# Kernel tuning notes

Measured on AMD Instinct MI355X. Metric: run time of the kernel, lower is better.

## Reference

```python
import jax, jax.numpy as jnp
import numpy as np

H = W = 256          # full-res feature map (2h x 2w)
WIN = 16             # window size
STRIDE = 2           # shifted-window stride
HEADS = 8
DIM_HEAD = 64
INNER = HEADS * DIM_HEAD
DIM = 128
KEEP = 50            # min(int(0.7*(256//16)**2), 50)
IOU_THR = 0.2


def _make_windows():
    xs = np.arange(0, W - WIN + 1, STRIDE)
    ys = np.arange(0, H - WIN + 1, STRIDE)
    gx, gy = np.meshgrid(xs, ys)
    return np.stack([gx.ravel(), gy.ravel(), gx.ravel() + WIN - 1, gy.ravel() + WIN - 1], axis=1)

_WIN_NP = _make_windows()          # [M,4] = (x1,y1,x2,y2), M = 121*121 = 14641
BOXES = jnp.asarray(_WIN_NP, dtype=jnp.float32)
SXY = jnp.asarray(_WIN_NP[:, :2], dtype=jnp.int32)   # integer (sx, sy) origins

# torchvision roi_align (spatial_scale=1, sampling_ratio->ceil(15/16)=1, aligned=False):
_off = (np.arange(WIN) + 0.5) * (WIN - 1.0) / WIN
LO = jnp.asarray(np.floor(_off).astype(np.int32))      # low integer index, in [0,14]
FR = jnp.asarray((_off - np.floor(_off)).astype(np.float32))


def _nms_keep(scores):
    """Greedy NMS over the fixed window grid; returns top-KEEP kept indices."""
    x1, y1, x2, y2 = BOXES[:, 0], BOXES[:, 1], BOXES[:, 2], BOXES[:, 3]
    area = (x2 - x1) * (y2 - y1)

    def body(k, carry):
        live, keep = carry
        idx = jnp.argmax(jnp.where(live, scores, -jnp.inf))
        bb = BOXES[idx]
        iw = jnp.clip(jnp.minimum(x2, bb[2]) - jnp.maximum(x1, bb[0]), 0.0)
        ih = jnp.clip(jnp.minimum(y2, bb[3]) - jnp.maximum(y1, bb[1]), 0.0)
        inter = iw * ih
        iou = inter / (area + area[idx] - inter)
        live = live & (iou <= IOU_THR)
        return live, keep.at[k].set(idx.astype(jnp.int32))

    _, keep = jax.lax.fori_loop(
        0, KEEP, body,
        (jnp.ones(BOXES.shape[0], bool), jnp.zeros(KEEP, jnp.int32)))
    return keep


def _forward(x, prob, fix_w, w_qkv, w_out, b_out):
    b = prob.shape[0]
    d = x.shape[-1]
    # entropy map at half res
    entropy = -jnp.sum(prob * jnp.log2(prob + 1e-10), axis=1)          # [b,128,128]
    # FixCNN: 8x8 ones-init conv, VALID -> [b,1,121,121]; normalized window score
    score = jax.lax.conv_general_dilated(
        entropy[:, None], fix_w, (1, 1), 'VALID',
        dimension_numbers=('NCHW', 'OIHW', 'NCHW'))
    score = score.reshape(b, -1) / float((WIN // 2) * (WIN // 2))      # [b,14641]

    keep = jax.lax.stop_gradient(jax.vmap(_nms_keep)(score))           # [b,KEEP]
    sx = SXY[keep][..., 0]                                             # [b,KEEP]
    sy = SXY[keep][..., 1]

    x2d = x.reshape(b, H, W, d)   # token n = h*W + w (channels-last layout)
    ar = jnp.arange(WIN)

    def gather_one(xi, syi, sxi):  # xi [H,W,d]
        R = syi[:, None, None] + ar[None, :, None]
        C = sxi[:, None, None] + ar[None, None, :]
        return xi[R, C]

    crops = jax.vmap(gather_one)(x2d, sy, sx)                          # [b,K,16,16,d]

    # roi_align bilinear sampling with fixed fractional grid
    c00 = crops[:, :, LO[:, None], LO[None, :]]
    c01 = crops[:, :, LO[:, None], LO[None, :] + 1]
    c10 = crops[:, :, LO[:, None] + 1, LO[None, :]]
    c11 = crops[:, :, LO[:, None] + 1, LO[None, :] + 1]
    fy = FR[:, None, None]
    fx = FR[None, :, None]
    win = ((1 - fy) * (1 - fx) * c00 + (1 - fy) * fx * c01
           + fy * (1 - fx) * c10 + fy * fx * c11)                      # [b,K,16,16,d]

    toks = win.reshape(b * KEEP, WIN * WIN, d)                         # [m,256,d]
    qkv = toks @ w_qkv.T                                               # [m,256,3*INNER]
    q, k_, v = jnp.split(qkv, 3, axis=-1)

    def to_heads(t):
        return t.reshape(t.shape[0], t.shape[1], HEADS, DIM_HEAD).transpose(0, 2, 1, 3)

    q, k_, v = to_heads(q), to_heads(k_), to_heads(v)
    attn = jax.nn.softmax(jnp.einsum('mhnd,mhkd->mhnk', q, k_) * (DIM_HEAD ** -0.5), axis=-1)
    out = jnp.einsum('mhnk,mhkd->mhnd', attn, v)
    out = out.transpose(0, 2, 1, 3).reshape(b * KEEP, WIN * WIN, INNER)
    out = out @ w_out.T + b_out                                        # [m,256,d]

    # overlap scatter-add + count normalization
    out2d = out.reshape(b, KEEP, WIN, WIN, d)
    bidx = jnp.arange(b)[:, None, None, None]
    Y = sy[:, :, None, None] + ar[None, None, :, None]
    X = sx[:, :, None, None] + ar[None, None, None, :]
    acc = jnp.zeros((b, H, W, d), x.dtype).at[bidx, Y, X].add(out2d)
    cnt = jnp.zeros((b, H, W), x.dtype).at[bidx, Y, X].add(1.0)
    outx = (acc / (cnt[..., None] + 1e-10)).reshape(b, H * W, d)
    return x + outx


def setup_inputs() -> dict:
    key = jax.random.key(0)
    ks = jax.random.split(key, 4)
    b = 4
    x = jax.random.normal(ks[0], (b, H * W, DIM), dtype=jnp.float32)
    prob = jax.random.uniform(ks[1], (b, 2, H // 2, W // 2), dtype=jnp.float32)
    fix_w = jnp.ones((1, 1, WIN // 2, WIN // 2), dtype=jnp.float32)
    w_qkv = jax.random.normal(ks[2], (3 * INNER, DIM), dtype=jnp.float32) * 0.02
    w_out = jax.random.normal(ks[3], (DIM, INNER), dtype=jnp.float32) * 0.02
    b_out = jnp.zeros((DIM,), dtype=jnp.float32)
    return {"x": x, "prob": prob, "fix_w": fix_w, "w_qkv": w_qkv, "w_out": w_out, "b_out": b_out}


def reference(x, prob, fix_w, w_qkv, w_out, b_out):
    return _forward(x, prob, fix_w, w_qkv, w_out, b_out)
```

## Files before the change

kernel.cpp:

```cpp
#include <hip/hip_runtime.h>
#include <math.h>

#define NB 4
#define NWIN 121
#define NBOX (NWIN*NWIN)
#define NKEEP 50
#define HWD 256
#define DIM 128
#define HEADS 8
#define NTOK 256
#define NWTOT (NB*NKEEP)
#define SCPAD 15616

#define OFF_ENT   0
#define OFF_SCORE 65536
#define OFF_KEEP  128128
#define OFF_WQKV  128256
#define OFF_WOUT  226560
#define OFF_TOKBF 259328
#define OFF_PO    3536128
#define WS_FLOATS 6812928

#define KPAD 76
#define VPAD 268
#define KP3 68
#define VP3 132

typedef __attribute__((ext_vector_type(8))) short short8;
typedef __attribute__((ext_vector_type(4))) short short4v;
typedef __attribute__((ext_vector_type(4))) float f32x4;

static __device__ __forceinline__ unsigned short f2bf(float f) {
  union { float f; unsigned u; } v; v.f = f;
  unsigned r = (v.u + 0x7fffu + ((v.u >> 16) & 1u)) >> 16;
  return (unsigned short)r;
}
static __device__ __forceinline__ short4v pk4(f32x4 a) {
  short4v r;
  r[0] = (short)f2bf(a[0]); r[1] = (short)f2bf(a[1]);
  r[2] = (short)f2bf(a[2]); r[3] = (short)f2bf(a[3]);
  return r;
}
static __device__ __forceinline__ short8 ld8_lds(const unsigned short* p) {
  short4v a = *(const short4v*)p;
  short4v b = *(const short4v*)(p + 4);
  short8 r;
  r[0]=a[0]; r[1]=a[1]; r[2]=a[2]; r[3]=a[3];
  r[4]=b[0]; r[5]=b[1]; r[6]=b[2]; r[7]=b[3];
  return r;
}
static __device__ __forceinline__ short8 ld8_g(const unsigned short* p) {
  return *(const short8*)p;
}

template<int CTRL>
static __device__ __forceinline__ float dppmax(float v) {
  union { float f; int i; } a, r; a.f = v;
  r.i = __builtin_amdgcn_update_dpp(a.i, a.i, CTRL, 0xf, 0xf, false);
  return fmaxf(v, r.f);
}
static __device__ __forceinline__ float wavemax(float v) {
  v = dppmax<0x111>(v); v = dppmax<0x112>(v);
  v = dppmax<0x114>(v); v = dppmax<0x118>(v);
  v = dppmax<0x142>(v); v = dppmax<0x143>(v);
  union { float f; int i; } gi, gm; gi.f = v;
  gm.i = __builtin_amdgcn_readlane(gi.i, 63);
  return gm.f;
}

__global__ void k_entropy(const float* __restrict__ prob, float* __restrict__ ent) {
  int idx = blockIdx.x * 256 + threadIdx.x;
  int b = idx >> 14, p = idx & 16383;
  float p0 = prob[(size_t)(b * 2) * 16384 + p];
  float p1 = prob[(size_t)(b * 2 + 1) * 16384 + p];
  ent[idx] = -(p0 * log2f(p0 + 1e-10f) + p1 * log2f(p1 + 1e-10f));
}

__global__ void k_score(const float* __restrict__ ent, const float* __restrict__ fw,
                        float* __restrict__ scp) {
  int gid = blockIdx.x * 256 + threadIdx.x;
  if (gid >= NB * SCPAD) return;
  int b = gid / SCPAD, idx = gid % SCPAD;
  int r = idx >> 7, c = idx & 127;
  float s = -INFINITY;
  if (r < NWIN && c < NWIN) {
    const float* e = ent + b * 16384 + r * 128 + c;
    float a = 0.f;
#pragma unroll
    for (int rr = 0; rr < 8; ++rr)
#pragma unroll
      for (int cc = 0; cc < 8; ++cc)
        a += e[rr * 128 + cc] * fw[rr * 8 + cc];
    s = a * (1.0f / 64.0f);
  }
  scp[b * SCPAD + (r << 7) + (c ^ ((r & 7) << 2))] = s;
}

__global__ void k_nms(const float* __restrict__ scp, int* __restrict__ keep) {
  __shared__ float sc[SCPAD];
  int b = blockIdx.x, l = threadIdx.x;
  const float* src = scp + b * SCPAD;
  for (int cb = 0; cb < 64; cb += 8) {
    f32x4 t[8];
#pragma unroll
    for (int i = 0; i < 8; ++i) {
      int idx = (cb + i) * 256 + l * 4;
      if (idx < SCPAD) t[i] = *(const f32x4*)&src[idx];
    }
#pragma unroll
    for (int i = 0; i < 8; ++i) {
      int idx = (cb + i) * 256 + l * 4;
      if (idx < SCPAD) *(f32x4*)&sc[idx] = t[i];
    }
  }
  float M0 = -INFINITY, M1 = -INFINITY; int C0 = 0, C1 = 0;
#pragma unroll
  for (int slot = 0; slot < 2; ++slot) {
    int r = l + slot * 64;
    if (slot == 1 && r >= NWIN) break;
    int r7 = (r & 7) << 2, rbase = r << 7;
    float bv0=-INFINITY,bv1=-INFINITY,bv2=-INFINITY,bv3=-INFINITY;
    int bc0=0,bc1=0,bc2=0,bc3=0;
    for (int lb = 0; lb < 32; ++lb) {
      f32x4 v = *(const f32x4*)&sc[rbase + ((lb << 2) ^ r7)];
      int c0 = lb << 2;
      if (v[0] > bv0) { bv0 = v[0]; bc0 = c0; }
      if (v[1] > bv1) { bv1 = v[1]; bc1 = c0 + 1; }
      if (v[2] > bv2) { bv2 = v[2]; bc2 = c0 + 2; }
      if (v[3] > bv3) { bv3 = v[3]; bc3 = c0 + 3; }
    }
    float bv = bv0; int bc = bc0;
    if (bv1 > bv || (bv1 == bv && bc1 < bc)) { bv = bv1; bc = bc1; }
    if (bv2 > bv || (bv2 == bv && bc2 < bc)) { bv = bv2; bc = bc2; }
    if (bv3 > bv || (bv3 == bv && bc3 < bc)) { bv = bv3; bc = bc3; }
    if (slot == 0) { M0 = bv; C0 = bc; } else { M1 = bv; C1 = bc; }
  }
  for (int k = 0; k < NKEEP; ++k) {
    float gmax = wavemax(fmaxf(M0, M1));
    unsigned long long b0 = __ballot(M0 == gmax);
    unsigned long long b1 = __ballot(M1 == gmax);
    int R;
    if (b0) R = __ffsll((unsigned long long)b0) - 1;
    else    R = 64 + __ffsll((unsigned long long)b1) - 1;
    int Cc = (R < 64) ? __builtin_amdgcn_readlane(C0, R)
                      : __builtin_amdgcn_readlane(C1, R - 64);
    if (l == 0) {
      keep[(b * NKEEP + k) * 2 + 0] = 2 * R;
      keep[(b * NKEEP + k) * 2 + 1] = 2 * Cc;
    }
    bool kill0 = false, kill1 = false;
    {
      int dy = l - R, ady = dy < 0 ? -dy : dy;
      if (ady <= 4) {
        int ih = 15 - 2 * ady;
#pragma unroll
        for (int dx = -4; dx <= 4; ++dx) {
          int adx = dx < 0 ? -dx : dx;
          if ((15 - 2 * adx) * ih > 75) {
            int cc = Cc + dx;
            if ((unsigned)cc < (unsigned)NWIN)
              sc[(l << 7) + (cc ^ ((l & 7) << 2))] = -INFINITY;
          }
        }
        int adx = C0 - Cc; adx = adx < 0 ? -adx : adx;
        kill0 = (adx <= 4) && ((15 - 2 * adx) * ih > 75);
      }
    }
    if (l + 64 < NWIN) {
      int r1 = l + 64;
      int dy = r1 - R, ady = dy < 0 ? -dy : dy;
      if (ady <= 4) {
        int ih = 15 - 2 * ady;
#pragma unroll
        for (int dx = -4; dx <= 4; ++dx) {
          int adx = dx < 0 ? -dx : dx;
          if ((15 - 2 * adx) * ih > 75) {
            int cc = Cc + dx;
            if ((unsigned)cc < (unsigned)NWIN)
              sc[(r1 << 7) + (cc ^ ((r1 & 7) << 2))] = -INFINITY;
          }
        }
        int adx = C1 - Cc; adx = adx < 0 ? -adx : adx;
        kill1 = (adx <= 4) && ((15 - 2 * adx) * ih > 75);
      }
    }
    unsigned long long need0 = __ballot(kill0);
    unsigned long long need1 = __ballot(kill1);
    while (need0 | need1) {
      int rr;
      if (need0) { rr = __ffsll((unsigned long long)need0) - 1; need0 &= need0 - 1; }
      else       { rr = __ffsll((unsigned long long)need1) - 1 + 64; need1 &= need1 - 1; }
      int r7 = (rr & 7) << 2, rbase = rr << 7;
      float v0 = sc[rbase + (l ^ r7)];
      float v1 = sc[rbase + ((l + 64) ^ r7)];
      float rmax = wavemax(fmaxf(v0, v1));
      unsigned long long e0 = __ballot(v0 == rmax);
      unsigned long long e1 = __ballot(v1 == rmax);
      int bc;
      if (e0) bc = __ffsll((unsigned long long)e0) - 1;
      else    bc = 64 + __ffsll((unsigned long long)e1) - 1;
      if (l == (rr & 63)) {
        if (rr >= 64) { M1 = rmax; C1 = bc; }
        else          { M0 = rmax; C0 = bc; }
      }
    }
  }
}

__global__ void k_wcvt(const float* __restrict__ wqkv, const float* __restrict__ wout,
                       unsigned short* __restrict__ wqkv_bf, unsigned short* __restrict__ wout_bf) {
  int i = blockIdx.x * 256 + threadIdx.x;
  if (i < 196608) wqkv_bf[i] = f2bf(wqkv[i]);
  int j = i - 196608;
  if (j >= 0 && j < 65536) wout_bf[j] = f2bf(wout[j]);
}

__global__ void k_toks(const float* __restrict__ x, const int* __restrict__ keep,
                       unsigned short* __restrict__ tokbf) {
  int w = blockIdx.x;
  int b = w / NKEEP;
  int sy = keep[w * 2 + 0], sx = keep[w * 2 + 1];
  int tid = threadIdx.x;
  int ch = tid & 127, th = tid >> 7;
  const float* xb = x + (size_t)b * 65536 * DIM;
  for (int it = 0; it < 128; ++it) {
    int tk = it * 2 + th;
    int i = tk >> 4, j = tk & 15;
    float offy = (i + 0.5f) * 0.9375f;
    float offx = (j + 0.5f) * 0.9375f;
    int li = (int)offy, lj = (int)offx;
    float fy = offy - (float)li, fx = offx - (float)lj;
    const float* p = xb + ((size_t)((sy + li) * HWD + (sx + lj))) * DIM + ch;
    float v00 = p[0], v01 = p[DIM], v10 = p[HWD * DIM], v11 = p[HWD * DIM + DIM];
    float w00 = (1.f - fy) * (1.f - fx), w01 = (1.f - fy) * fx;
    float w10 = fy * (1.f - fx), w11 = fy * fx;
    tokbf[((size_t)w * NTOK + tk) * DIM + ch] = f2bf(w00 * v00 + w01 * v01 + w10 * v10 + w11 * v11);
  }
}

__global__ __launch_bounds__(512, 2) void k_attn3(
    const unsigned short* __restrict__ tokbf,
    const unsigned short* __restrict__ wqkv,
    const unsigned short* __restrict__ wout,
    unsigned short* __restrict__ po) {
  __shared__ __align__(16) char smem[55296];
  unsigned short* Kh  = (unsigned short*)smem;
  unsigned short* VTh = (unsigned short*)(smem + 17408);
  const int tid = threadIdx.x;
  const int wv = tid >> 6, ln = tid & 63, lo = ln & 15, hi = ln >> 4;
  const int bid = blockIdx.x;
  const int win = bid >> 1, qh = bid & 1;
  unsigned short* QP = (unsigned short*)(smem + 34304 + wv * 2176);
  const unsigned short* tw = tokbf + (size_t)win * NTOK * DIM;
  const int qb = qh * 128 + wv * 16;

  f32x4 pacc[8];
#pragma unroll
  for (int mf = 0; mf < 8; ++mf) pacc[mf] = (f32x4){0.f,0.f,0.f,0.f};

  for (int h = 0; h < HEADS; ++h) {
    {
      f32x4 qacc[4];
#pragma unroll
      for (int mf = 0; mf < 4; ++mf) qacc[mf] = (f32x4){0.f,0.f,0.f,0.f};
#pragma unroll
      for (int kf = 0; kf < 4; ++kf) {
        short8 bt = ld8_g(&tw[(qb + lo) * 128 + kf * 32 + hi * 8]);
#pragma unroll
        for (int mf = 0; mf < 4; ++mf) {
          short8 aw = ld8_g(wqkv + (size_t)(h * 64 + mf * 16 + lo) * 128 + kf * 32 + hi * 8);
          qacc[mf] = __builtin_amdgcn_mfma_f32_16x16x32_bf16(aw, bt, qacc[mf], 0, 0, 0);
        }
      }
#pragma unroll
      for (int mf = 0; mf < 4; ++mf)
        *(short4v*)&QP[lo * KP3 + mf * 16 + hi * 4] = pk4(qacc[mf] * 0.125f);
    }
    short8 Qb[2];
#pragma unroll
    for (int kf = 0; kf < 2; ++kf)
      Qb[kf] = ld8_lds(&QP[lo * KP3 + kf * 32 + hi * 8]);

    f32x4 Ot[4];
#pragma unroll
    for (int mf = 0; mf < 4; ++mf) Ot[mf] = (f32x4){0.f,0.f,0.f,0.f};
    float mrow = -INFINITY, lrow = 0.f;

    for (int half = 0; half < 2; ++half) {
      __syncthreads();
      const int kbase = half * 128 + wv * 16;
      {
        f32x4 kacc[4];
#pragma unroll
        for (int mf = 0; mf < 4; ++mf) kacc[mf] = (f32x4){0.f,0.f,0.f,0.f};
#pragma unroll
        for (int kf = 0; kf < 4; ++kf) {
          short8 bt = ld8_g(&tw[(kbase + lo) * 128 + kf * 32 + hi * 8]);
#pragma unroll
          for (int mf = 0; mf < 4; ++mf) {
            short8 aw = ld8_g(wqkv + (size_t)(512 + h * 64 + mf * 16 + lo) * 128 + kf * 32 + hi * 8);
            kacc[mf] = __builtin_amdgcn_mfma_f32_16x16x32_bf16(aw, bt, kacc[mf], 0, 0, 0);
          }
        }
#pragma unroll
        for (int mf = 0; mf < 4; ++mf)
          *(short4v*)&Kh[(wv * 16 + lo) * KP3 + mf * 16 + hi * 4] = pk4(kacc[mf]);
      }
      {
        f32x4 vacc[4];
#pragma unroll
        for (int nf = 0; nf < 4; ++nf) vacc[nf] = (f32x4){0.f,0.f,0.f,0.f};
#pragma unroll
        for (int kf = 0; kf < 4; ++kf) {
          short8 at = ld8_g(&tw[(kbase + lo) * 128 + kf * 32 + hi * 8]);
#pragma unroll
          for (int nf = 0; nf < 4; ++nf) {
            short8 bw = ld8_g(wqkv + (size_t)(1024 + h * 64 + nf * 16 + lo) * 128 + kf * 32 + hi * 8);
            vacc[nf] = __builtin_amdgcn_mfma_f32_16x16x32_bf16(at, bw, vacc[nf], 0, 0, 0);
          }
        }
#pragma unroll
        for (int nf = 0; nf < 4; ++nf)
          *(short4v*)&VTh[(nf * 16 + lo) * VP3 + wv * 16 + hi * 4] = pk4(vacc[nf]);
      }
      __syncthreads();

      for (int ck = 0; ck < 2; ++ck) {
        f32x4 sacc[4];
#pragma unroll
        for (int mf = 0; mf < 4; ++mf) sacc[mf] = (f32x4){0.f,0.f,0.f,0.f};
#pragma unroll
        for (int kf = 0; kf < 2; ++kf) {
          short8 ka[4];
#pragma unroll
          for (int mf = 0; mf < 4; ++mf)
            ka[mf] = ld8_lds(&Kh[(ck * 64 + mf * 16 + lo) * KP3 + kf * 32 + hi * 8]);
#pragma unroll
          for (int mf = 0; mf < 4; ++mf)
            sacc[mf] = __builtin_amdgcn_mfma_f32_16x16x32_bf16(ka[mf], Qb[kf], sacc[mf], 0, 0, 0);
        }

        float cmax = -INFINITY;
#pragma unroll
        for (int mf = 0; mf < 4; ++mf)
#pragma unroll
          for (int r = 0; r < 4; ++r) cmax = fmaxf(cmax, sacc[mf][r]);
        cmax = fmaxf(cmax, __shfl_xor(cmax, 16));
        cmax = fmaxf(cmax, __shfl_xor(cmax, 32));
        float mnew = fmaxf(mrow, cmax);
        float corr = __expf(mrow - mnew);
        float ps = 0.f;
#pragma unroll
        for (int mf = 0; mf < 4; ++mf)
#pragma unroll
          for (int r = 0; r < 4; ++r) {
            float e = __expf(sacc[mf][r] - mnew);
            sacc[mf][r] = e; ps += e;
          }
        ps += __shfl_xor(ps, 16);
        ps += __shfl_xor(ps, 32);
        lrow = lrow * corr + ps;
        mrow = mnew;
#pragma unroll
        for (int mf = 0; mf < 4; ++mf) Ot[mf] *= corr;

#pragma unroll
        for (int mf = 0; mf < 4; ++mf)
          *(short4v*)&QP[lo * KP3 + mf * 16 + hi * 4] = pk4(sacc[mf]);
        short8 pb[2];
#pragma unroll
        for (int kf = 0; kf < 2; ++kf)
          pb[kf] = ld8_lds(&QP[lo * KP3 + kf * 32 + hi * 8]);
#pragma unroll
        for (int kf = 0; kf < 2; ++kf) {
          short8 va[4];
#pragma unroll
          for (int mf = 0; mf < 4; ++mf)
            va[mf] = ld8_lds(&VTh[(mf * 16 + lo) * VP3 + ck * 64 + kf * 32 + hi * 8]);
#pragma unroll
          for (int mf = 0; mf < 4; ++mf)
            Ot[mf] = __builtin_amdgcn_mfma_f32_16x16x32_bf16(va[mf], pb[kf], Ot[mf], 0, 0, 0);
        }
      }
    }

    {
      float inv = 1.f / lrow;
#pragma unroll
      for (int mf = 0; mf < 4; ++mf)
        *(short4v*)&QP[lo * KP3 + mf * 16 + hi * 4] = pk4(Ot[mf] * inv);
    }
    short8 Ob[2];
#pragma unroll
    for (int kf = 0; kf < 2; ++kf)
      Ob[kf] = ld8_lds(&QP[lo * KP3 + kf * 32 + hi * 8]);
#pragma unroll
    for (int kf = 0; kf < 2; ++kf) {
#pragma unroll
      for (int mh = 0; mh < 2; ++mh) {
        short8 aw[4];
#pragma unroll
        for (int m4 = 0; m4 < 4; ++m4)
          aw[m4] = ld8_g(wout + (size_t)((mh * 4 + m4) * 16 + lo) * 512 + h * 64 + kf * 32 + hi * 8);
#pragma unroll
        for (int m4 = 0; m4 < 4; ++m4)
          pacc[mh * 4 + m4] = __builtin_amdgcn_mfma_f32_16x16x32_bf16(aw[m4], Ob[kf], pacc[mh * 4 + m4], 0, 0, 0);
      }
    }
  }

#pragma unroll
  for (int mf = 0; mf < 8; ++mf)
    *(short4v*)&po[((size_t)win * NTOK + qb + lo) * 128 + mf * 16 + hi * 4] = pk4(pacc[mf]);
}

__global__ __launch_bounds__(512, 2) void k_attn(
    const unsigned short* __restrict__ tokbf,
    const unsigned short* __restrict__ wqkv,
    const unsigned short* __restrict__ wout,
    unsigned short* __restrict__ po) {
  __shared__ __align__(16) char smem[112128];
  unsigned short* Klds = (unsigned short*)smem;
  unsigned short* VT   = (unsigned short*)(smem + 38912);
  const int tid = threadIdx.x;
  const int wv = tid >> 6, ln = tid & 63;
  const int lo = ln & 15, hi = ln >> 4;
  const int win = blockIdx.x;
  unsigned short* QP = (unsigned short*)(smem + 73216 + wv * 4864);
  const unsigned short* tw = tokbf + (size_t)win * NTOK * DIM;
  const int qrow = wv * 32;

  f32x4 pacc[8][2];
#pragma unroll
  for (int mf = 0; mf < 8; ++mf)
#pragma unroll
    for (int nf = 0; nf < 2; ++nf) pacc[mf][nf] = (f32x4){0.f,0.f,0.f,0.f};

  for (int h = 0; h < HEADS; ++h) {
    if (h) __syncthreads();
    {
      f32x4 kacc[4][2];
#pragma unroll
      for (int mf = 0; mf < 4; ++mf)
#pragma unroll
        for (int nf = 0; nf < 2; ++nf) kacc[mf][nf] = (f32x4){0.f,0.f,0.f,0.f};
#pragma unroll
      for (int kf = 0; kf < 4; ++kf) {
        short8 aw[4], bt[2];
#pragma unroll
        for (int mf = 0; mf < 4; ++mf)
          aw[mf] = ld8_g(wqkv + (size_t)(512 + h * 64 + mf * 16 + lo) * 128 + kf * 32 + hi * 8);
#pragma unroll
        for (int nf = 0; nf < 2; ++nf)
          bt[nf] = ld8_g(&tw[(qrow + nf * 16 + lo) * 128 + kf * 32 + hi * 8]);
#pragma unroll
        for (int mf = 0; mf < 4; ++mf)
#pragma unroll
          for (int nf = 0; nf < 2; ++nf)
            kacc[mf][nf] = __builtin_amdgcn_mfma_f32_16x16x32_bf16(aw[mf], bt[nf], kacc[mf][nf], 0, 0, 0);
      }
#pragma unroll
      for (int mf = 0; mf < 4; ++mf)
#pragma unroll
        for (int nf = 0; nf < 2; ++nf)
          *(short4v*)&Klds[(qrow + nf * 16 + lo) * KPAD + mf * 16 + hi * 4] = pk4(kacc[mf][nf]);
    }
    {
      f32x4 vacc[2][4];
#pragma unroll
      for (int mf = 0; mf < 2; ++mf)
#pragma unroll
        for (int nf = 0; nf < 4; ++nf) vacc[mf][nf] = (f32x4){0.f,0.f,0.f,0.f};
#pragma unroll
      for (int kf = 0; kf < 4; ++kf) {
        short8 at[2], bw[4];
#pragma unroll
        for (int mf = 0; mf < 2; ++mf)
          at[mf] = ld8_g(&tw[(qrow + mf * 16 + lo) * 128 + kf * 32 + hi * 8]);
#pragma unroll
        for (int nf = 0; nf < 4; ++nf)
          bw[nf] = ld8_g(wqkv + (size_t)(1024 + h * 64 + nf * 16 + lo) * 128 + kf * 32 + hi * 8);
#pragma unroll
        for (int mf = 0; mf < 2; ++mf)
#pragma unroll
          for (int nf = 0; nf < 4; ++nf)
            vacc[mf][nf] = __builtin_amdgcn_mfma_f32_16x16x32_bf16(at[mf], bw[nf], vacc[mf][nf], 0, 0, 0);
      }
#pragma unroll
      for (int mf = 0; mf < 2; ++mf)
#pragma unroll
        for (int nf = 0; nf < 4; ++nf)
          *(short4v*)&VT[(nf * 16 + lo) * VPAD + qrow + mf * 16 + hi * 4] = pk4(vacc[mf][nf]);
    }
    {
      f32x4 qacc[4][2];
#pragma unroll
      for (int mf = 0; mf < 4; ++mf)
#pragma unroll
        for (int nf = 0; nf < 2; ++nf) qacc[mf][nf] = (f32x4){0.f,0.f,0.f,0.f};
#pragma unroll
      for (int kf = 0; kf < 4; ++kf) {
        short8 aw[4], bt[2];
#pragma unroll
        for (int mf = 0; mf < 4; ++mf)
          aw[mf] = ld8_g(wqkv + (size_t)(h * 64 + mf * 16 + lo) * 128 + kf * 32 + hi * 8);
#pragma unroll
        for (int nf = 0; nf < 2; ++nf)
          bt[nf] = ld8_g(&tw[(qrow + nf * 16 + lo) * 128 + kf * 32 + hi * 8]);
#pragma unroll
        for (int mf = 0; mf < 4; ++mf)
#pragma unroll
          for (int nf = 0; nf < 2; ++nf)
            qacc[mf][nf] = __builtin_amdgcn_mfma_f32_16x16x32_bf16(aw[mf], bt[nf], qacc[mf][nf], 0, 0, 0);
      }
#pragma unroll
      for (int mf = 0; mf < 4; ++mf)
#pragma unroll
        for (int nf = 0; nf < 2; ++nf)
          *(short4v*)&QP[(nf * 16 + lo) * KPAD + mf * 16 + hi * 4] = pk4(qacc[mf][nf] * 0.125f);
    }
    __syncthreads();

    short8 Qb[2][2];
#pragma unroll
    for (int nf = 0; nf < 2; ++nf)
#pragma unroll
      for (int kf = 0; kf < 2; ++kf)
        Qb[nf][kf] = ld8_lds(&QP[(nf * 16 + lo) * KPAD + kf * 32 + hi * 8]);

    f32x4 Ot[4][2];
#pragma unroll
    for (int mf = 0; mf < 4; ++mf)
#pragma unroll
      for (int nf = 0; nf < 2; ++nf) Ot[mf][nf] = (f32x4){0.f,0.f,0.f,0.f};
    float mrow[2] = {-INFINITY, -INFINITY};
    float lrow[2] = {0.f, 0.f};

    for (int ck = 0; ck < 4; ++ck) {
      f32x4 sacc[4][2];
#pragma unroll
      for (int mf = 0; mf < 4; ++mf)
#pragma unroll
        for (int nf = 0; nf < 2; ++nf) sacc[mf][nf] = (f32x4){0.f,0.f,0.f,0.f};
      short8 ka[4][2];
#pragma unroll
      for (int mf = 0; mf < 4; ++mf)
#pragma unroll
        for (int kf = 0; kf < 2; ++kf)
          ka[mf][kf] = ld8_lds(&Klds[(ck * 64 + mf * 16 + lo) * KPAD + kf * 32 + hi * 8]);
#pragma unroll
      for (int mf = 0; mf < 4; ++mf)
#pragma unroll
        for (int nf = 0; nf < 2; ++nf)
#pragma unroll
          for (int kf = 0; kf < 2; ++kf)
            sacc[mf][nf] = __builtin_amdgcn_mfma_f32_16x16x32_bf16(ka[mf][kf], Qb[nf][kf], sacc[mf][nf], 0, 0, 0);

#pragma unroll
      for (int nf = 0; nf < 2; ++nf) {
        float cmax = -INFINITY;
#pragma unroll
        for (int mf = 0; mf < 4; ++mf)
#pragma unroll
          for (int r = 0; r < 4; ++r) cmax = fmaxf(cmax, sacc[mf][nf][r]);
        cmax = fmaxf(cmax, __shfl_xor(cmax, 16));
        cmax = fmaxf(cmax, __shfl_xor(cmax, 32));
        float mnew = fmaxf(mrow[nf], cmax);
        float corr = __expf(mrow[nf] - mnew);
        float ps = 0.f;
#pragma unroll
        for (int mf = 0; mf < 4; ++mf)
#pragma unroll
          for (int r = 0; r < 4; ++r) {
            float e = __expf(sacc[mf][nf][r] - mnew);
            sacc[mf][nf][r] = e; ps += e;
          }
        ps += __shfl_xor(ps, 16);
        ps += __shfl_xor(ps, 32);
        lrow[nf] = lrow[nf] * corr + ps;
        mrow[nf] = mnew;
#pragma unroll
        for (int mf = 0; mf < 4; ++mf) Ot[mf][nf] *= corr;
      }
#pragma unroll
      for (int mf = 0; mf < 4; ++mf)
#pragma unroll
        for (int nf = 0; nf < 2; ++nf)
          *(short4v*)&QP[(nf * 16 + lo) * KPAD + mf * 16 + hi * 4] = pk4(sacc[mf][nf]);
      short8 pb[2][2], va[4][2];
#pragma unroll
      for (int nf = 0; nf < 2; ++nf)
#pragma unroll
        for (int kf = 0; kf < 2; ++kf)
          pb[nf][kf] = ld8_lds(&QP[(nf * 16 + lo) * KPAD + kf * 32 + hi * 8]);
#pragma unroll
      for (int mf = 0; mf < 4; ++mf)
#pragma unroll
        for (int kf = 0; kf < 2; ++kf)
          va[mf][kf] = ld8_lds(&VT[(mf * 16 + lo) * VPAD + ck * 64 + kf * 32 + hi * 8]);
#pragma unroll
      for (int mf = 0; mf < 4; ++mf)
#pragma unroll
        for (int nf = 0; nf < 2; ++nf)
#pragma unroll
          for (int kf = 0; kf < 2; ++kf)
            Ot[mf][nf] = __builtin_amdgcn_mfma_f32_16x16x32_bf16(va[mf][kf], pb[nf][kf], Ot[mf][nf], 0, 0, 0);
    }

#pragma unroll
    for (int nf = 0; nf < 2; ++nf) {
      float inv = 1.f / lrow[nf];
#pragma unroll
      for (int mf = 0; mf < 4; ++mf)
        *(short4v*)&QP[(nf * 16 + lo) * KPAD + mf * 16 + hi * 4] = pk4(Ot[mf][nf] * inv);
    }
    short8 Ob[2][2];
#pragma unroll
    for (int nf = 0; nf < 2; ++nf)
#pragma unroll
      for (int kf = 0; kf < 2; ++kf)
        Ob[nf][kf] = ld8_lds(&QP[(nf * 16 + lo) * KPAD + kf * 32 + hi * 8]);
#pragma unroll
    for (int kf = 0; kf < 2; ++kf) {
      short8 aw[8];
#pragma unroll
      for (int mf = 0; mf < 8; ++mf)
        aw[mf] = ld8_g(wout + (size_t)(mf * 16 + lo) * 512 + h * 64 + kf * 32 + hi * 8);
#pragma unroll
      for (int mf = 0; mf < 8; ++mf)
#pragma unroll
        for (int nf = 0; nf < 2; ++nf)
          pacc[mf][nf] = __builtin_amdgcn_mfma_f32_16x16x32_bf16(aw[mf], Ob[nf][kf], pacc[mf][nf], 0, 0, 0);
    }
  }
#pragma unroll
  for (int mf = 0; mf < 8; ++mf)
#pragma unroll
    for (int nf = 0; nf < 2; ++nf)
      *(short4v*)&po[((size_t)win * NTOK + qrow + nf * 16 + lo) * 128 + mf * 16 + hi * 4] = pk4(pacc[mf][nf]);
}

__global__ void k_final(const float* __restrict__ x, const unsigned short* __restrict__ po,
                        const int* __restrict__ keep, const float* __restrict__ bout,
                        float* __restrict__ out) {
  __shared__ int kp[2 * NKEEP];
  int tid = threadIdx.x;
  int gid = blockIdx.x * 256 + tid;
  int chq = gid & 3, pix = gid >> 2;
  int b = pix >> 16, pb = pix & 65535, y = pb >> 8, xx = pb & 255;
  if (tid < 2 * NKEEP) kp[tid] = keep[b * 2 * NKEEP + tid];
  __syncthreads();
  float acc[32];
#pragma unroll
  for (int i = 0; i < 32; ++i) acc[i] = 0.f;
  float cnt = 0.f;
  for (int w = 0; w < NKEEP; ++w) {
    int dy = y - kp[2 * w], dx = xx - kp[2 * w + 1];
    if ((unsigned)dy < 16u && (unsigned)dx < 16u) {
      cnt += 1.f;
      const unsigned short* pp = po + ((size_t)(b * NKEEP + w) * NTOK + dy * 16 + dx) * 128 + chq * 32;
#pragma unroll
      for (int k2 = 0; k2 < 4; ++k2) {
        short8 v = ld8_g(pp + k2 * 8);
#pragma unroll
        for (int j = 0; j < 8; ++j) {
          union { unsigned u; float f; } cv;
          cv.u = ((unsigned)(unsigned short)v[j]) << 16;
          acc[k2 * 8 + j] += cv.f;
        }
      }
    }
  }
  size_t base = (size_t)pix * 128 + chq * 32;
  float inv = 1.f / (cnt + 1e-10f);
#pragma unroll
  for (int i = 0; i < 32; ++i)
    out[base + i] = x[base + i] + (acc[i] + cnt * bout[chq * 32 + i]) * inv;
}

extern "C" void kernel_launch(void* const* d_in, const int* in_sizes, int n_in,
                              void* d_out, int out_size, void* d_ws, size_t ws_size,
                              hipStream_t stream) {
  const float* x    = (const float*)d_in[0];
  const float* prob = (const float*)d_in[1];
  const float* fixw = (const float*)d_in[2];
  const float* wqkv = (const float*)d_in[3];
  const float* wout = (const float*)d_in[4];
  const float* bout = (const float*)d_in[5];
  float* out = (float*)d_out;
  float* ws  = (float*)d_ws;
  if (ws_size < (size_t)WS_FLOATS * 4) return;

  float* ent  = ws + OFF_ENT;
  float* scp  = ws + OFF_SCORE;
  int*   keep = (int*)(ws + OFF_KEEP);
  unsigned short* wqkv_bf = (unsigned short*)(ws + OFF_WQKV);
  unsigned short* wout_bf = (unsigned short*)(ws + OFF_WOUT);
  unsigned short* tokbf   = (unsigned short*)(ws + OFF_TOKBF);
  unsigned short* po      = (unsigned short*)(ws + OFF_PO);

  hipFuncAttributes fa;
  int use3 = 0;
  if (hipFuncGetAttributes(&fa, (const void*)k_attn3) == hipSuccess)
    use3 = (fa.localSizeBytes == 0) && (fa.numRegs <= 128);

  k_entropy<<<256, 256, 0, stream>>>(prob, ent);
  k_score<<<(NB * SCPAD + 255) / 256, 256, 0, stream>>>(ent, fixw, scp);
  k_wcvt<<<1024, 256, 0, stream>>>(wqkv, wout, wqkv_bf, wout_bf);
  k_nms<<<NB, 64, 0, stream>>>(scp, keep);
  k_toks<<<NWTOT, 256, 0, stream>>>(x, keep, tokbf);
  if (use3)
    k_attn3<<<NWTOT * 2, 512, 0, stream>>>(tokbf, wqkv_bf, wout_bf, po);
  else
    k_attn<<<NWTOT, 512, 0, stream>>>(tokbf, wqkv_bf, wout_bf, po);
  k_final<<<NB * 65536 * 4 / 256, 256, 0, stream>>>(x, po, keep, bout, out);
}
```

Measured before the change: 390.4 us.

## Split output projection out of attention kernel into separate GEMM kernel

The attention kernel no longer accumulates the per-head output projection in registers. It now writes normalized per-head attention outputs (bf16, all 512 inner channels) to a new global workspace buffer. A new k_proj kernel then runs the 512x128 output projection as one dense MFMA GEMM per window. The block index order is also changed so both query halves of a window sit in different grid halves. This frees registers and the per-head projection loop in the attention kernel, but adds an extra global round trip of about 50 MB and another launch. It also needs a larger workspace, falling back to the old unsplit kernel otherwise.

```diff
diff --git a/kernel.cpp b/kernel.cpp
--- a/kernel.cpp
+++ b/kernel.cpp
@@ -20,6 +20,8 @@
 #define OFF_TOKBF 259328
 #define OFF_PO    3536128
 #define WS_FLOATS 6812928
+#define OFF_KG    6812928
+#define OG_FLOATS 13107200
 
 #define KPAD 76
 #define VPAD 268
@@ -238,25 +240,20 @@
   }
 }
 
-__global__ __launch_bounds__(512, 2) void k_attn3(
+__global__ __launch_bounds__(512, 2) void k_attn5(
     const unsigned short* __restrict__ tokbf,
     const unsigned short* __restrict__ wqkv,
-    const unsigned short* __restrict__ wout,
-    unsigned short* __restrict__ po) {
+    unsigned short* __restrict__ Og) {
   __shared__ __align__(16) char smem[55296];
   unsigned short* Kh  = (unsigned short*)smem;
   unsigned short* VTh = (unsigned short*)(smem + 17408);
   const int tid = threadIdx.x;
   const int wv = tid >> 6, ln = tid & 63, lo = ln & 15, hi = ln >> 4;
   const int bid = blockIdx.x;
-  const int win = bid >> 1, qh = bid & 1;
+  const int win = bid % NWTOT, qh = bid / NWTOT;
   unsigned short* QP = (unsigned short*)(smem + 34304 + wv * 2176);
   const unsigned short* tw = tokbf + (size_t)win * NTOK * DIM;
   const int qb = qh * 128 + wv * 16;
-
-  f32x4 pacc[8];
-#pragma unroll
-  for (int mf = 0; mf < 8; ++mf) pacc[mf] = (f32x4){0.f,0.f,0.f,0.f};
 
   for (int h = 0; h < HEADS; ++h) {
     {
@@ -388,30 +385,47 @@
       float inv = 1.f / lrow;
 #pragma unroll
       for (int mf = 0; mf < 4; ++mf)
-        *(short4v*)&QP[lo * KP3 + mf * 16 + hi * 4] = pk4(Ot[mf] * inv);
-    }
-    short8 Ob[2];
-#pragma unroll
-    for (int kf = 0; kf < 2; ++kf)
-      Ob[kf] = ld8_lds(&QP[lo * KP3 + kf * 32 + hi * 8]);
-#pragma unroll
-    for (int kf = 0; kf < 2; ++kf) {
-#pragma unroll
-      for (int mh = 0; mh < 2; ++mh) {
-        short8 aw[4];
-#pragma unroll
-        for (int m4 = 0; m4 < 4; ++m4)
-          aw[m4] = ld8_g(wout + (size_t)((mh * 4 + m4) * 16 + lo) * 512 + h * 64 + kf * 32 + hi * 8);
-#pragma unroll
-        for (int m4 = 0; m4 < 4; ++m4)
-          pacc[mh * 4 + m4] = __builtin_amdgcn_mfma_f32_16x16x32_bf16(aw[m4], Ob[kf], pacc[mh * 4 + m4], 0, 0, 0);
-      }
-    }
-  }
-
+        *(short4v*)&Og[((size_t)win * 256 + qb + lo) * 512 + h * 64 + mf * 16 + hi * 4]
+          = pk4(Ot[mf] * inv);
+    }
+  }
+}
+
+__global__ __launch_bounds__(512, 2) void k_proj(
+    const unsigned short* __restrict__ Oall,
+    const unsigned short* __restrict__ wout,
+    unsigned short* __restrict__ po) {
+  int lw = blockIdx.x;
+  int tid = threadIdx.x;
+  int wv = tid >> 6, ln = tid & 63, lo = ln & 15, hi = ln >> 4;
+  int qb = wv * 32;
+  const unsigned short* Ob = Oall + (size_t)lw * 131072;
+  f32x4 pacc[8][2];
 #pragma unroll
   for (int mf = 0; mf < 8; ++mf)
-    *(short4v*)&po[((size_t)win * NTOK + qb + lo) * 128 + mf * 16 + hi * 4] = pk4(pacc[mf]);
+#pragma unroll
+    for (int nf = 0; nf < 2; ++nf) pacc[mf][nf] = (f32x4){0.f,0.f,0.f,0.f};
+#pragma unroll
+  for (int kf = 0; kf < 16; ++kf) {
+    short8 aw[8], bt[2];
+#pragma unroll
+    for (int mf = 0; mf < 8; ++mf)
+      aw[mf] = ld8_g(wout + (size_t)(mf * 16 + lo) * 512 + kf * 32 + hi * 8);
+#pragma unroll
+    for (int nf = 0; nf < 2; ++nf)
+      bt[nf] = ld8_g(&Ob[(qb + nf * 16 + lo) * 512 + kf * 32 + hi * 8]);
+#pragma unroll
+    for (int mf = 0; mf < 8; ++mf)
+#pragma unroll
+      for (int nf = 0; nf < 2; ++nf)
+        pacc[mf][nf] = __builtin_amdgcn_mfma_f32_16x16x32_bf16(aw[mf], bt[nf], pacc[mf][nf], 0, 0, 0);
+  }
+#pragma unroll
+  for (int mf = 0; mf < 8; ++mf)
+#pragma unroll
+    for (int nf = 0; nf < 2; ++nf)
+      *(short4v*)&po[((size_t)lw * NTOK + qb + nf * 16 + lo) * 128 + mf * 16 + hi * 4]
+        = pk4(pacc[mf][nf]);
 }
 
 __global__ __launch_bounds__(512, 2) void k_attn(
@@ -699,19 +713,26 @@
   unsigned short* tokbf   = (unsigned short*)(ws + OFF_TOKBF);
   unsigned short* po      = (unsigned short*)(ws + OFF_PO);
 
-  hipFuncAttributes fa;
-  int use3 = 0;
-  if (hipFuncGetAttributes(&fa, (const void*)k_attn3) == hipSuccess)
-    use3 = (fa.localSizeBytes == 0) && (fa.numRegs <= 128);
+  int use5 = (ws_size >= ((size_t)OFF_KG + OG_FLOATS) * 4);
+  if (use5) {
+    hipFuncAttributes fa;
+    if (hipFuncGetAttributes(&fa, (const void*)k_attn5) == hipSuccess)
+      use5 = (fa.localSizeBytes == 0) && (fa.numRegs <= 128);
+    else
+      use5 = 0;
+  }
 
   k_entropy<<<256, 256, 0, stream>>>(prob, ent);
   k_score<<<(NB * SCPAD + 255) / 256, 256, 0, stream>>>(ent, fixw, scp);
   k_wcvt<<<1024, 256, 0, stream>>>(wqkv, wout, wqkv_bf, wout_bf);
   k_nms<<<NB, 64, 0, stream>>>(scp, keep);
   k_toks<<<NWTOT, 256, 0, stream>>>(x, keep, tokbf);
-  if (use3)
-    k_attn3<<<NWTOT * 2, 512, 0, stream>>>(tokbf, wqkv_bf, wout_bf, po);
-  else
+  if (use5) {
+    unsigned short* Og = (unsigned short*)(ws + OFF_KG);
+    k_attn5<<<NWTOT * 2, 512, 0, stream>>>(tokbf, wqkv_bf, Og);
+    k_proj<<<NWTOT, 512, 0, stream>>>(Og, wout_bf, po);
+  } else {
     k_attn<<<NWTOT, 512, 0, stream>>>(tokbf, wqkv_bf, wout_bf, po);
+  }
   k_final<<<NB * 65536 * 4 / 256, 256, 0, stream>>>(x, po, keep, bout, out);
 }
```

Result: no change. 390.6 us (+0.0%).
